# Kernel optimization log

Hardware: AMD Instinct MI355X
Metric: run time of the kernel (lower is better)

Reference implementation:

```python
import math
import jax, jax.numpy as jnp
import numpy as np

D_MODEL = 1024
N_HEAD = 16
D_K = D_MODEL // N_HEAD  # 64
D_V = D_MODEL // N_HEAD  # 64


def setup_inputs() -> dict:
    key = jax.random.key(0)
    kx, kq, kk, kv, ko = jax.random.split(key, 5)
    B, L = 4, 2048
    x = jax.random.normal(kx, (B, L, D_MODEL), dtype=jnp.float32)
    mask = jnp.zeros((B, 1, 1, L), dtype=bool)  # True = masked; all-False here
    s = 1.0 / math.sqrt(D_MODEL)
    # torch nn.Linear weights: shape (out_features, in_features), y = x @ W.T
    Wq = jax.random.normal(kq, (D_K * N_HEAD, D_MODEL), dtype=jnp.float32) * s
    Wk = jax.random.normal(kk, (D_K * N_HEAD, D_MODEL), dtype=jnp.float32) * s
    Wv = jax.random.normal(kv, (D_V * N_HEAD, D_MODEL), dtype=jnp.float32) * s
    Wo = jax.random.normal(ko, (D_MODEL, D_V * N_HEAD), dtype=jnp.float32) * s
    return {"x": x, "mask": mask, "Wq": Wq, "Wk": Wk, "Wv": Wv, "Wo": Wo}


def reference(x, mask, Wq, Wk, Wv, Wo):
    B, L, D = x.shape
    H, Dh, Dv = N_HEAD, D_K, D_V
    # projections (torch Linear: x @ W.T), then split heads -> (B,H,L,Dh)
    q = (x @ Wq.T).reshape(B, L, H, Dh).transpose(0, 2, 1, 3)
    k = (x @ Wk.T).reshape(B, L, H, Dh).transpose(0, 2, 1, 3)
    v = (x @ Wv.T).reshape(B, L, H, Dv).transpose(0, 2, 1, 3)
    scores = jnp.einsum('bhqd,bhkd->bhqk', q, k) / math.sqrt(Dh)
    scores = jnp.where(mask, -jnp.inf, scores)
    attn = jax.nn.softmax(scores, axis=-1)  # dropout p=0.0 -> identity
    out = jnp.einsum('bhqk,bhkd->bhqd', attn, v)  # (B,H,L,Dv)
    out = out.transpose(0, 2, 1, 3).reshape(B, L, H * Dv)
    return out @ Wo.T
```

## Files before the change

kernel.cpp:

```cpp
#include <hip/hip_runtime.h>

typedef __bf16 bf16_t;
typedef __bf16 bf16x4 __attribute__((ext_vector_type(4)));
typedef __bf16 bf16x8 __attribute__((ext_vector_type(8)));
typedef float f32x4 __attribute__((ext_vector_type(4)));

#define MFMA_16x16x32 __builtin_amdgcn_mfma_f32_16x16x32_bf16

#define GLD16(dst_lds, src_glb) \
  __builtin_amdgcn_global_load_lds((__attribute__((address_space(1))) void*)(void*)(src_glb), \
                                   (__attribute__((address_space(3))) void*)(dst_lds), 16, 0, 0)

#define EXP2RAW __builtin_amdgcn_exp2f

#define QSCALE 0.18033688011112042f

__global__ void cvt_all(const float* __restrict__ x,  const float* __restrict__ wq,
                        const float* __restrict__ wk, const float* __restrict__ wv,
                        const float* __restrict__ wo,
                        bf16_t* __restrict__ xb, bf16_t* __restrict__ wqkv,
                        bf16_t* __restrict__ wob) {
    const int XN = 8 * 1024 * 1024, WN = 1024 * 1024;
    int i = (blockIdx.x * blockDim.x + threadIdx.x) * 4;
    const float* s; bf16_t* d; int off;
    if (i < XN)                { s = x;  d = xb;            off = i; }
    else if (i < XN + WN)      { s = wq; d = wqkv;          off = i - XN; }
    else if (i < XN + 2 * WN)  { s = wk; d = wqkv + WN;     off = i - XN - WN; }
    else if (i < XN + 3 * WN)  { s = wv; d = wqkv + 2 * WN; off = i - XN - 2 * WN; }
    else                       { s = wo; d = wob;           off = i - XN - 3 * WN; }
    float4 v = *(const float4*)(s + off);
    bf16x4 o;
    o[0] = (bf16_t)v.x; o[1] = (bf16_t)v.y; o[2] = (bf16_t)v.z; o[3] = (bf16_t)v.w;
    *(bf16x4*)(d + off) = o;
}

__global__ __launch_bounds__(256) void gemm_qkv(
    const bf16_t* __restrict__ A, const bf16_t* __restrict__ W,
    bf16_t* __restrict__ qo, bf16_t* __restrict__ ko, bf16_t* __restrict__ vto)
{
    constexpr int K = 1024, BK = 64;
    __shared__ bf16_t smem[16896];
    bf16_t* As = smem;
    bf16_t* Bs = smem + 8192;
    const int t = threadIdx.x;
    const int lane = t & 63, wave = t >> 6;
    const int quad = lane >> 4, l16 = lane & 15;
    const int m0 = blockIdx.x * 128, n0 = blockIdx.y * 128;
    const int wm = (wave & 1) * 64, wn = (wave >> 1) * 64;

    f32x4 acc[4][4] = {};

    int goff[4];
#pragma unroll
    for (int m = 0; m < 4; ++m) {
        int c = t + m * 256;
        int row = c >> 3;
        goff[m] = row * K + (((c & 7) ^ (row & 7)) * 8);
    }

    for (int k0 = 0; k0 < K; k0 += BK) {
        __syncthreads();
#pragma unroll
        for (int m = 0; m < 4; ++m) {
            int c8 = (t + m * 256) * 8;
            GLD16(As + c8, A + (size_t)m0 * K + k0 + goff[m]);
            GLD16(Bs + c8, W + (size_t)n0 * K + k0 + goff[m]);
        }
        __syncthreads();
#pragma unroll
        for (int half = 0; half < 2; ++half) {
            const int sw = (((half * 4 + quad) ^ (l16 & 7)) * 8);
            bf16x8 af[4], bfr[4];
#pragma unroll
            for (int i = 0; i < 4; ++i)
                af[i] = *(const bf16x8*)(As + (wm + i * 16 + l16) * 64 + sw);
#pragma unroll
            for (int j = 0; j < 4; ++j)
                bfr[j] = *(const bf16x8*)(Bs + (wn + j * 16 + l16) * 64 + sw);
#pragma unroll
            for (int i = 0; i < 4; ++i)
#pragma unroll
                for (int j = 0; j < 4; ++j)
                    acc[i][j] = MFMA_16x16x32(af[i], bfr[j], acc[i][j], 0, 0, 0);
        }
    }

    if (n0 < 2048) {
#pragma unroll
        for (int i = 0; i < 4; ++i) {
#pragma unroll
            for (int j = 0; j < 4; ++j) {
#pragma unroll
                for (int r = 0; r < 4; ++r) {
                    int row = m0 + wm + i * 16 + quad * 4 + r;
                    int col = n0 + wn + j * 16 + l16;
                    float v = acc[i][j][r];
                    int b = row >> 11, l = row & 2047;
                    int sec = col >> 10, c2 = col & 1023;
                    int h = c2 >> 6, dd = c2 & 63;
                    size_t bh = (size_t)b * 16 + h;
                    if (sec == 0) qo[(bh * 2048 + l) * 64 + dd] = (bf16_t)(v * QSCALE);
                    else          ko[(bh * 2048 + l) * 64 + dd] = (bf16_t)v;
                }
            }
        }
    } else {
        __syncthreads();
        const int hh = wave >> 1;
#pragma unroll
        for (int i = 0; i < 4; ++i) {
            int lbase = wm + (i >> 1) * 32;
            int slot0 = quad * 8 + (i & 1) * 4;
#pragma unroll
            for (int j = 0; j < 4; ++j) {
                int dd = j * 16 + l16;
                bf16x4 pk;
#pragma unroll
                for (int r = 0; r < 4; ++r) pk[r] = (bf16_t)acc[i][j][r];
                *(bf16x4*)(smem + (hh * 64 + dd) * 132 + lbase + slot0) = pk;
            }
        }
        __syncthreads();
        const int b = m0 >> 11, lb = m0 & 2047;
        const int h0 = (n0 - 2048) >> 6;
#pragma unroll
        for (int r8 = 0; r8 < 8; ++r8) {
            int c = r8 * 256 + t;
            int ch = c >> 10, cc = c & 1023;
            int dd = cc >> 4, lc = (cc & 15) * 8;
            bf16x8 vv = *(const bf16x8*)(smem + (ch * 64 + dd) * 132 + lc);
            size_t bh = (size_t)b * 16 + h0 + ch;
            *(bf16x8*)(vto + (bh * 64 + dd) * 2048 + lb + lc) = vv;
        }
    }
}

__global__ __launch_bounds__(256) void gemm_out(
    const bf16_t* __restrict__ A, const bf16_t* __restrict__ W,
    float* __restrict__ out)
{
    constexpr int K = 1024, BK = 64;
    __shared__ bf16_t smem[16384];
    bf16_t* As = smem;
    bf16_t* Bs = smem + 8192;
    const int t = threadIdx.x;
    const int lane = t & 63, wave = t >> 6;
    const int quad = lane >> 4, l16 = lane & 15;
    const int m0 = blockIdx.x * 128, n0 = blockIdx.y * 128;
    const int wm = (wave & 1) * 64, wn = (wave >> 1) * 64;

    f32x4 acc[4][4] = {};

    int goff[4];
#pragma unroll
    for (int m = 0; m < 4; ++m) {
        int c = t + m * 256;
        int row = c >> 3;
        goff[m] = row * K + (((c & 7) ^ (row & 7)) * 8);
    }

    for (int k0 = 0; k0 < K; k0 += BK) {
        __syncthreads();
#pragma unroll
        for (int m = 0; m < 4; ++m) {
            int c8 = (t + m * 256) * 8;
            GLD16(As + c8, A + (size_t)m0 * K + k0 + goff[m]);
            GLD16(Bs + c8, W + (size_t)n0 * K + k0 + goff[m]);
        }
        __syncthreads();
#pragma unroll
        for (int half = 0; half < 2; ++half) {
            const int sw = (((half * 4 + quad) ^ (l16 & 7)) * 8);
            bf16x8 af[4], bfr[4];
#pragma unroll
            for (int i = 0; i < 4; ++i)
                af[i] = *(const bf16x8*)(As + (wm + i * 16 + l16) * 64 + sw);
#pragma unroll
            for (int j = 0; j < 4; ++j)
                bfr[j] = *(const bf16x8*)(Bs + (wn + j * 16 + l16) * 64 + sw);
#pragma unroll
            for (int i = 0; i < 4; ++i)
#pragma unroll
                for (int j = 0; j < 4; ++j)
                    acc[i][j] = MFMA_16x16x32(af[i], bfr[j], acc[i][j], 0, 0, 0);
        }
    }

#pragma unroll
    for (int i = 0; i < 4; ++i)
#pragma unroll
        for (int j = 0; j < 4; ++j)
#pragma unroll
            for (int r = 0; r < 4; ++r) {
                int row = m0 + wm + i * 16 + quad * 4 + r;
                int col = n0 + wn + j * 16 + l16;
                out[(size_t)row * 1024 + col] = acc[i][j][r];
            }
}

__global__ __launch_bounds__(256, 2) void attn(
    const bf16_t* __restrict__ q, const bf16_t* __restrict__ k,
    const bf16_t* __restrict__ vt, bf16_t* __restrict__ ho)
{
    constexpr int L = 2048, DH = 64;
    const int bid = blockIdx.x;
    const int bh = bid & 63, qblk = bid >> 6;
    const bf16_t* Q   = q  + (size_t)bh * L * DH;
    const bf16_t* Kg  = k  + (size_t)bh * L * DH;
    const bf16_t* VTg = vt + (size_t)bh * L * DH;
    const int t = threadIdx.x, lane = t & 63, wave = t >> 6;
    const int quad = lane >> 4, l16 = lane & 15;
    const int qrow0 = qblk * 256 + wave * 64;

    __shared__ bf16_t Ks[4][2][2048];
    __shared__ bf16_t Vs[4][2][2048];

    const bf16_t* kga[4];
    const bf16_t* vga[4];
#pragma unroll
    for (int i = 0; i < 4; ++i) {
        int c = i * 64 + lane;
        int slg = (((c & 3) ^ ((c >> 3) & 3)) * 8);
        kga[i] = Kg  + (size_t)((c >> 2) & 31) * DH + (c >> 7) * 32 + slg;
        vga[i] = VTg + (size_t)((c >> 2) & 63) * L + slg;
    }

    bf16x8 bq[4][2];
#pragma unroll
    for (int s4 = 0; s4 < 4; ++s4) {
        bq[s4][0] = *(const bf16x8*)(Q + (size_t)(qrow0 + s4 * 16 + l16) * DH + quad * 8);
        bq[s4][1] = *(const bf16x8*)(Q + (size_t)(qrow0 + s4 * 16 + l16) * DH + 32 + quad * 8);
    }

    bf16x8 vone;
#pragma unroll
    for (int e = 0; e < 8; ++e) vone[e] = (bf16_t)1.0f;

    f32x4 o[4][4] = {};
    f32x4 lsacc[4] = {};

    const int ksw = ((quad ^ ((l16 >> 1) & 3)) * 8);

#pragma unroll
    for (int i = 0; i < 4; ++i) {
        GLD16(&Ks[wave][0][0] + (i * 64 + lane) * 8, kga[i]);
        GLD16(&Vs[wave][0][0] + (i * 64 + lane) * 8, vga[i]);
    }

    for (int ic = 0; ic < 64; ++ic) {
        const int buf = ic & 1;
        const bf16_t* kb = &Ks[wave][buf][0];
        const bf16_t* vb = &Vs[wave][buf][0];
        if (ic + 1 < 64) {
            bf16_t* kn = &Ks[wave][buf ^ 1][0];
            bf16_t* vn = &Vs[wave][buf ^ 1][0];
            const size_t ko = (size_t)(ic + 1) * 32 * DH;
            const int vo = (ic + 1) * 32;
#pragma unroll
            for (int i = 0; i < 4; ++i) {
                GLD16(kn + (i * 64 + lane) * 8, kga[i] + ko);
                GLD16(vn + (i * 64 + lane) * 8, vga[i] + vo);
            }
            asm volatile("s_waitcnt vmcnt(8)" ::: "memory");
        } else {
            asm volatile("s_waitcnt vmcnt(0)" ::: "memory");
        }
        __builtin_amdgcn_sched_barrier(0);

        bf16x8 ak[2][2];
#pragma unroll
        for (int ss = 0; ss < 2; ++ss) {
            ak[ss][0] = *(const bf16x8*)(kb + (ss * 16 + l16) * 32 + ksw);
            ak[ss][1] = *(const bf16x8*)(kb + 1024 + (ss * 16 + l16) * 32 + ksw);
        }
        f32x4 st[4][2];
        __builtin_amdgcn_s_setprio(1);
#pragma unroll
        for (int q4 = 0; q4 < 4; ++q4)
#pragma unroll
            for (int ss = 0; ss < 2; ++ss) {
                f32x4 z = {};
                z = MFMA_16x16x32(ak[ss][0], bq[q4][0], z, 0, 0, 0);
                st[q4][ss] = MFMA_16x16x32(ak[ss][1], bq[q4][1], z, 0, 0, 0);
            }
        __builtin_amdgcn_s_setprio(0);

        bf16x8 p[4];
#pragma unroll
        for (int q4 = 0; q4 < 4; ++q4)
#pragma unroll
            for (int r = 0; r < 4; ++r) {
                float e0 = EXP2RAW(st[q4][0][r]);
                float e1 = EXP2RAW(st[q4][1][r]);
                p[q4][r]     = (bf16_t)e0;
                p[q4][4 + r] = (bf16_t)e1;
            }

        __builtin_amdgcn_s_setprio(1);
#pragma unroll
        for (int q4 = 0; q4 < 4; ++q4)
            lsacc[q4] = MFMA_16x16x32(vone, p[q4], lsacc[q4], 0, 0, 0);
#pragma unroll
        for (int tt = 0; tt < 4; ++tt) {
            bf16x8 av = *(const bf16x8*)(vb + (tt * 16 + l16) * 32 + ksw);
#pragma unroll
            for (int q4 = 0; q4 < 4; ++q4)
                o[q4][tt] = MFMA_16x16x32(av, p[q4], o[q4][tt], 0, 0, 0);
        }
        __builtin_amdgcn_s_setprio(0);
    }

    const int b = bh >> 4, hd = bh & 15;
#pragma unroll
    for (int q4 = 0; q4 < 4; ++q4) {
        const float inv = 1.0f / lsacc[q4][0];
        const int tok = b * 2048 + qrow0 + q4 * 16 + l16;
#pragma unroll
        for (int tt = 0; tt < 4; ++tt) {
            bf16x4 ov;
#pragma unroll
            for (int r = 0; r < 4; ++r) ov[r] = (bf16_t)(o[q4][tt][r] * inv);
            *(bf16x4*)(ho + (size_t)tok * 1024 + hd * 64 + tt * 16 + quad * 4) = ov;
        }
    }
}

extern "C" void kernel_launch(void* const* d_in, const int* in_sizes, int n_in,
                              void* d_out, int out_size, void* d_ws, size_t ws_size,
                              hipStream_t stream) {
    const float* x  = (const float*)d_in[0];
    const float* Wq = (const float*)d_in[2];
    const float* Wk = (const float*)d_in[3];
    const float* Wv = (const float*)d_in[4];
    const float* Wo = (const float*)d_in[5];
    float* out = (float*)d_out;

    bf16_t* ws   = (bf16_t*)d_ws;
    bf16_t* xb   = ws;
    bf16_t* wqkv = xb   + (size_t)8192 * 1024;
    bf16_t* wob  = wqkv + (size_t)3072 * 1024;
    bf16_t* qb   = wob  + (size_t)1024 * 1024;
    bf16_t* kb   = qb   + (size_t)8192 * 1024;
    bf16_t* vtb  = kb   + (size_t)8192 * 1024;
    bf16_t* hob  = vtb  + (size_t)8192 * 1024;

    cvt_all<<<12288, 256, 0, stream>>>(x, Wq, Wk, Wv, Wo, xb, wqkv, wob);
    gemm_qkv<<<dim3(64, 24), 256, 0, stream>>>(xb, wqkv, qb, kb, vtb);
    attn<<<512, 256, 0, stream>>>(qb, kb, vtb, hob);
    gemm_out<<<dim3(64, 8), 256, 0, stream>>>(hob, wob, out);
}
```

Baseline: 253.0 us.

## Unroll attention K/V loop by two and interleave exp with QK MFMAs

Restructures the per-wave attention loop to process two K/V chunks per iteration. K and V fragments are loaded into registers early, and chunk B's QK^T MFMAs are interleaved with chunk A's exp2 work so the matrix and vector units overlap. The global-to-LDS prefetch of the next chunk is reissued as soon as the current buffer has been read into registers. This raises register pressure and adds explicit lgkmcnt waits, and the removed sched_barrier gives the compiler more freedom to reorder.

```diff
diff --git a/kernel.cpp b/kernel.cpp
--- a/kernel.cpp
+++ b/kernel.cpp
@@ -246,67 +246,131 @@
         GLD16(&Ks[wave][0][0] + (i * 64 + lane) * 8, kga[i]);
         GLD16(&Vs[wave][0][0] + (i * 64 + lane) * 8, vga[i]);
     }
-
-    for (int ic = 0; ic < 64; ++ic) {
-        const int buf = ic & 1;
-        const bf16_t* kb = &Ks[wave][buf][0];
-        const bf16_t* vb = &Vs[wave][buf][0];
-        if (ic + 1 < 64) {
-            bf16_t* kn = &Ks[wave][buf ^ 1][0];
-            bf16_t* vn = &Vs[wave][buf ^ 1][0];
-            const size_t ko = (size_t)(ic + 1) * 32 * DH;
-            const int vo = (ic + 1) * 32;
+#pragma unroll
+    for (int i = 0; i < 4; ++i) {
+        GLD16(&Ks[wave][1][0] + (i * 64 + lane) * 8, kga[i] + 32 * DH);
+        GLD16(&Vs[wave][1][0] + (i * 64 + lane) * 8, vga[i] + 32);
+    }
+
+    for (int ib = 0; ib < 32; ++ib) {
+        const int A = 2 * ib;
+        const bf16_t* kbA = &Ks[wave][0][0];
+        const bf16_t* vbA = &Vs[wave][0][0];
+        const bf16_t* kbB = &Ks[wave][1][0];
+        const bf16_t* vbB = &Vs[wave][1][0];
+
+        asm volatile("s_waitcnt vmcnt(8)" ::: "memory");
+        bf16x8 akA[2][2], avA[4];
+#pragma unroll
+        for (int ss = 0; ss < 2; ++ss) {
+            akA[ss][0] = *(const bf16x8*)(kbA + (ss * 16 + l16) * 32 + ksw);
+            akA[ss][1] = *(const bf16x8*)(kbA + 1024 + (ss * 16 + l16) * 32 + ksw);
+        }
+#pragma unroll
+        for (int tt = 0; tt < 4; ++tt)
+            avA[tt] = *(const bf16x8*)(vbA + (tt * 16 + l16) * 32 + ksw);
+
+        f32x4 stA[4][2];
+        __builtin_amdgcn_s_setprio(1);
+#pragma unroll
+        for (int q4 = 0; q4 < 4; ++q4)
+#pragma unroll
+            for (int ss = 0; ss < 2; ++ss) {
+                f32x4 z = {};
+                z = MFMA_16x16x32(akA[ss][0], bq[q4][0], z, 0, 0, 0);
+                stA[q4][ss] = MFMA_16x16x32(akA[ss][1], bq[q4][1], z, 0, 0, 0);
+            }
+        __builtin_amdgcn_s_setprio(0);
+
+        if (ib < 31) {
+            asm volatile("s_waitcnt lgkmcnt(0)" ::: "memory");
+            const size_t koff = (size_t)(A + 2) * 32 * DH;
+            const int voff = (A + 2) * 32;
 #pragma unroll
             for (int i = 0; i < 4; ++i) {
-                GLD16(kn + (i * 64 + lane) * 8, kga[i] + ko);
-                GLD16(vn + (i * 64 + lane) * 8, vga[i] + vo);
+                GLD16(&Ks[wave][0][0] + (i * 64 + lane) * 8, kga[i] + koff);
+                GLD16(&Vs[wave][0][0] + (i * 64 + lane) * 8, vga[i] + voff);
             }
             asm volatile("s_waitcnt vmcnt(8)" ::: "memory");
         } else {
             asm volatile("s_waitcnt vmcnt(0)" ::: "memory");
         }
-        __builtin_amdgcn_sched_barrier(0);
-
-        bf16x8 ak[2][2];
+
+        bf16x8 akB[2][2], avB[4];
 #pragma unroll
         for (int ss = 0; ss < 2; ++ss) {
-            ak[ss][0] = *(const bf16x8*)(kb + (ss * 16 + l16) * 32 + ksw);
-            ak[ss][1] = *(const bf16x8*)(kb + 1024 + (ss * 16 + l16) * 32 + ksw);
-        }
-        f32x4 st[4][2];
+            akB[ss][0] = *(const bf16x8*)(kbB + (ss * 16 + l16) * 32 + ksw);
+            akB[ss][1] = *(const bf16x8*)(kbB + 1024 + (ss * 16 + l16) * 32 + ksw);
+        }
+#pragma unroll
+        for (int tt = 0; tt < 4; ++tt)
+            avB[tt] = *(const bf16x8*)(vbB + (tt * 16 + l16) * 32 + ksw);
+
+        bf16x8 pA[4];
+#pragma unroll
+        for (int q4 = 0; q4 < 4; ++q4)
+#pragma unroll
+            for (int r = 0; r < 4; ++r) {
+                float e0 = EXP2RAW(stA[q4][0][r]);
+                float e1 = EXP2RAW(stA[q4][1][r]);
+                pA[q4][r]     = (bf16_t)e0;
+                pA[q4][4 + r] = (bf16_t)e1;
+            }
+
+        f32x4 stB[4][2];
         __builtin_amdgcn_s_setprio(1);
 #pragma unroll
         for (int q4 = 0; q4 < 4; ++q4)
 #pragma unroll
             for (int ss = 0; ss < 2; ++ss) {
                 f32x4 z = {};
-                z = MFMA_16x16x32(ak[ss][0], bq[q4][0], z, 0, 0, 0);
-                st[q4][ss] = MFMA_16x16x32(ak[ss][1], bq[q4][1], z, 0, 0, 0);
+                z = MFMA_16x16x32(akB[ss][0], bq[q4][0], z, 0, 0, 0);
+                stB[q4][ss] = MFMA_16x16x32(akB[ss][1], bq[q4][1], z, 0, 0, 0);
             }
         __builtin_amdgcn_s_setprio(0);
 
-        bf16x8 p[4];
+        if (ib < 31) {
+            asm volatile("s_waitcnt lgkmcnt(0)" ::: "memory");
+            const size_t koff = (size_t)(A + 3) * 32 * DH;
+            const int voff = (A + 3) * 32;
+#pragma unroll
+            for (int i = 0; i < 4; ++i) {
+                GLD16(&Ks[wave][1][0] + (i * 64 + lane) * 8, kga[i] + koff);
+                GLD16(&Vs[wave][1][0] + (i * 64 + lane) * 8, vga[i] + voff);
+            }
+        }
+
+        __builtin_amdgcn_s_setprio(1);
+#pragma unroll
+        for (int q4 = 0; q4 < 4; ++q4)
+            lsacc[q4] = MFMA_16x16x32(vone, pA[q4], lsacc[q4], 0, 0, 0);
+#pragma unroll
+        for (int tt = 0; tt < 4; ++tt)
+#pragma unroll
+            for (int q4 = 0; q4 < 4; ++q4)
+                o[q4][tt] = MFMA_16x16x32(avA[tt], pA[q4], o[q4][tt], 0, 0, 0);
+        __builtin_amdgcn_s_setprio(0);
+
+        bf16x8 pB[4];
 #pragma unroll
         for (int q4 = 0; q4 < 4; ++q4)
 #pragma unroll
             for (int r = 0; r < 4; ++r) {
-                float e0 = EXP2RAW(st[q4][0][r]);
-                float e1 = EXP2RAW(st[q4][1][r]);
-                p[q4][r]     = (bf16_t)e0;
-                p[q4][4 + r] = (bf16_t)e1;
+                float e0 = EXP2RAW(stB[q4][0][r]);
+                float e1 = EXP2RAW(stB[q4][1][r]);
+                pB[q4][r]     = (bf16_t)e0;
+                pB[q4][4 + r] = (bf16_t)e1;
             }
 
         __builtin_amdgcn_s_setprio(1);
 #pragma unroll
         for (int q4 = 0; q4 < 4; ++q4)
-            lsacc[q4] = MFMA_16x16x32(vone, p[q4], lsacc[q4], 0, 0, 0);
-#pragma unroll
-        for (int tt = 0; tt < 4; ++tt) {
-            bf16x8 av = *(const bf16x8*)(vb + (tt * 16 + l16) * 32 + ksw);
+            lsacc[q4] = MFMA_16x16x32(vone, pB[q4], lsacc[q4], 0, 0, 0);
+#pragma unroll
+        for (int tt = 0; tt < 4; ++tt)
 #pragma unroll
             for (int q4 = 0; q4 < 4; ++q4)
-                o[q4][tt] = MFMA_16x16x32(av, p[q4], o[q4][tt], 0, 0, 0);
-        }
+                o[q4][tt] = MFMA_16x16x32(avB[tt], pB[q4], o[q4][tt], 0, 0, 0);
         __builtin_amdgcn_s_setprio(0);
     }
 
```

Result: no change. 252.4 us (-0.2%).
